# Optimization experiments

Measured on AMD Instinct MI355X. Metric: run time of the kernel, lower is better.

## Reference

```python
import jax, jax.numpy as jnp
import numpy as np


def setup_inputs() -> dict:
    key = jax.random.key(0)
    ks = jax.random.split(key, 6)
    B, T, I, H = 64, 4096, 128, 256
    x = jax.random.normal(ks[0], (B, T, I), dtype=jnp.float32)
    W_in = jax.random.normal(ks[1], (H, I), dtype=jnp.float32) * (1.0 / np.sqrt(I))
    b_in = jax.random.normal(ks[2], (H,), dtype=jnp.float32) * 0.01
    W_rec = jax.random.normal(ks[3], (H, H), dtype=jnp.float32) * (1.0 / np.sqrt(H))
    b_rec = jax.random.normal(ks[4], (H,), dtype=jnp.float32) * 0.01
    tau = jax.random.uniform(ks[5], (H,), dtype=jnp.float32)  # clamped to [0.1, 5] in forward
    return {"x": x, "W_in": W_in, "b_in": b_in, "W_rec": W_rec,
            "b_rec": b_rec, "tau": tau, "num_layers": 2}


def reference(x, W_in, b_in, W_rec, b_rec, tau, num_layers):
    # x: [B, T, I]; returns final hidden state h: [B, H]
    dt = jnp.float32(0.1)
    tau_c = jnp.clip(tau, 0.1, 5.0)                      # [H]
    scale = dt / tau_c                                   # [H]
    # Input projection is identical for every inner iteration -> precompute once.
    x_proj = jnp.einsum('bti,hi->bth', x, W_in) + b_in   # [B, T, H]
    B = x.shape[0]
    H = tau.shape[0]

    def step(h, xt):  # xt: [B, H]
        for _ in range(num_layers):  # small fixed inner loop
            act = jnp.tanh(xt + h @ W_rec.T + b_rec)
            h = h + scale * (act - h)
        return h, None

    h0 = jnp.zeros((B, H), dtype=x.dtype)
    h, _ = jax.lax.scan(step, h0, jnp.swapaxes(x_proj, 0, 1))  # scan over T
    return h
```

## Files before the change

kernel.cpp:

```cpp
#include <hip/hip_runtime.h>


typedef _Float16 half8 __attribute__((ext_vector_type(8)));
typedef float    f32x4 __attribute__((ext_vector_type(4)));

#define LGKM_BARRIER() asm volatile("s_waitcnt lgkmcnt(0)\n\ts_barrier" ::: "memory")

__device__ __forceinline__ half8 cvt8s(float4 v0, float4 v1, float s) {
    half8 hv;
    hv[0]=(_Float16)(v0.x*s); hv[1]=(_Float16)(v0.y*s);
    hv[2]=(_Float16)(v0.z*s); hv[3]=(_Float16)(v0.w*s);
    hv[4]=(_Float16)(v1.x*s); hv[5]=(_Float16)(v1.y*s);
    hv[6]=(_Float16)(v1.z*s); hv[7]=(_Float16)(v1.w*s);
    return hv;
}
__device__ __forceinline__ half8 cvt8(float4 v0, float4 v1) {
    half8 hv;
    hv[0]=(_Float16)v0.x; hv[1]=(_Float16)v0.y;
    hv[2]=(_Float16)v0.z; hv[3]=(_Float16)v0.w;
    hv[4]=(_Float16)v1.x; hv[5]=(_Float16)v1.y;
    hv[6]=(_Float16)v1.z; hv[7]=(_Float16)v1.w;
    return hv;
}

__global__ void __launch_bounds__(512, 2)
ltc_fused(const float* __restrict__ x,
          const float* __restrict__ W_in,
          const float* __restrict__ b_in,
          const float* __restrict__ W_rec,
          const float* __restrict__ b_rec,
          const float* __restrict__ tau,
          const int*   __restrict__ num_layers,
          float*       __restrict__ out,
          int T)
{
    const int b    = blockIdx.x;
    const int tid  = threadIdx.x;
    const int lane = tid & 63;
    const int g    = tid >> 6;
    const int n    = lane & 15;
    const int q    = lane >> 4;
    const int t_my = q & 1;
    const int L    = num_layers[0];
    const int mycol = 32*g + 16*t_my + n;
    const unsigned shamt = (unsigned)(t_my << 4);

    __shared__ _Float16 hbuf[2][256];
    __shared__ _Float16 xstage[2][16][16][8];
    __shared__ _Float16 pchunk[32][8][16][2];

    const float PRE = 2.8853900817779268f;
    half8 bh[2][8];
    half8 bx[2][4];
    float biasv[2];
#pragma unroll
    for (int t = 0; t < 2; ++t) {
        const int col = 32*g + 16*t + n;
        const float* rp = &W_rec[col * 256 + 8*q];
#pragma unroll
        for (int i = 0; i < 8; ++i)
            bh[t][i] = cvt8s(*(const float4*)&rp[32*i],
                             *(const float4*)&rp[32*i + 4], PRE);
        const float* ip = &W_in[col * 128 + 8*q];
#pragma unroll
        for (int i = 0; i < 4; ++i)
            bx[t][i] = cvt8s(*(const float4*)&ip[32*i],
                             *(const float4*)&ip[32*i + 4], PRE);
        biasv[t] = (b_in[col] + b_rec[col]) * PRE;
    }
    const float sj   = 0.1f / fminf(fmaxf(tau[mycol], 0.1f), 5.0f);
    const float nsj2 = -2.0f * sj;
    float hj = 0.0f;

    if (tid < 256) hbuf[0][tid] = (_Float16)0.0f;

    const float* xb  = x + (size_t)b * T * 128;
    const int    t_u = tid >> 4;
    const int    c16 = tid & 15;
    const int    Mts = t_u >> 4, ms = t_u & 15;

    float4 xpreA, xpreB;
    {
        int tg = t_u; if (tg > T - 1) tg = T - 1;
        const float4* src = (const float4*)(xb + (size_t)tg * 128 + 8*c16);
        xpreA = src[0]; xpreB = src[1];
    }

#define LAYER(RB, WB, XCQ)                                                   \
    do {                                                                     \
        half8 ah[8];                                                         \
        _Pragma("unroll")                                                    \
        for (int i = 0; i < 8; ++i)                                          \
            ah[i] = *(const half8*)&hbuf[RB][32*i + 8*q];                    \
        const float term1 = __builtin_fmaf(sj, 1.0f - hj, hj);               \
        const f32x4 zz = (f32x4){0.f, 0.f, 0.f, 0.f};                        \
        f32x4 A0[2], A1[2], A2[2], A3[2];                                    \
        _Pragma("unroll")                                                    \
        for (int t = 0; t < 2; ++t) {                                        \
            A0[t] = __builtin_amdgcn_mfma_f32_16x16x32_f16(                  \
                ah[0], bh[t][0], zz, 0, 0, 0);                               \
            A1[t] = __builtin_amdgcn_mfma_f32_16x16x32_f16(                  \
                ah[2], bh[t][2], zz, 0, 0, 0);                               \
            A2[t] = __builtin_amdgcn_mfma_f32_16x16x32_f16(                  \
                ah[4], bh[t][4], zz, 0, 0, 0);                               \
            A3[t] = __builtin_amdgcn_mfma_f32_16x16x32_f16(                  \
                ah[6], bh[t][6], zz, 0, 0, 0);                               \
        }                                                                    \
        _Pragma("unroll")                                                    \
        for (int t = 0; t < 2; ++t) {                                        \
            A0[t] = __builtin_amdgcn_mfma_f32_16x16x32_f16(                  \
                ah[1], bh[t][1], A0[t], 0, 0, 0);                            \
            A1[t] = __builtin_amdgcn_mfma_f32_16x16x32_f16(                  \
                ah[3], bh[t][3], A1[t], 0, 0, 0);                            \
            A2[t] = __builtin_amdgcn_mfma_f32_16x16x32_f16(                  \
                ah[5], bh[t][5], A2[t], 0, 0, 0);                            \
            A3[t] = __builtin_amdgcn_mfma_f32_16x16x32_f16(                  \
                ah[7], bh[t][7], A3[t], 0, 0, 0);                            \
        }                                                                    \
        float s0 = t_my ? A0[1][0] : A0[0][0];                               \
        float s1 = t_my ? A1[1][0] : A1[0][0];                               \
        float s2 = t_my ? A2[1][0] : A2[0][0];                               \
        float s3 = t_my ? A3[1][0] : A3[0][0];                               \
        float z  = ((s0 + s1) + (s2 + s3)) + (XCQ);                          \
        float e  = __builtin_amdgcn_exp2f(z);         \
        float rr = __builtin_amdgcn_rcpf(e + 1.0f);                          \
        hj = __builtin_fmaf(nsj2, rr, term1);            \
        hbuf[WB][mycol] = (_Float16)hj;  \
        LGKM_BARRIER();                                                      \
    } while (0)

#define STAGE_AND_PROJECT()                                                  \
    do {                                                                     \
        *(half8*)&xstage[Mts][c16][ms][0] = cvt8(xpreA, xpreB);              \
        __syncthreads();                                                     \
        _Pragma("unroll")                                                    \
        for (int Mt = 0; Mt < 2; ++Mt) {                                     \
            half8 ax[4];                                                     \
            _Pragma("unroll")                                                \
            for (int ks = 0; ks < 4; ++ks)                                   \
                ax[ks] = *(const half8*)&xstage[Mt][4*ks + q][n][0];         \
            f32x4 pa[2];                                                     \
            _Pragma("unroll")                                                \
            for (int t = 0; t < 2; ++t)                                      \
                pa[t] = (f32x4){biasv[t], biasv[t], biasv[t], biasv[t]};     \
            _Pragma("unroll")                                                \
            for (int ks = 0; ks < 4; ++ks)                                   \
                _Pragma("unroll")                                            \
                for (int t = 0; t < 2; ++t)                                  \
                    pa[t] = __builtin_amdgcn_mfma_f32_16x16x32_f16(          \
                        ax[ks], bx[t][ks], pa[t], 0, 0, 0);                  \
            _Pragma("unroll")                                                \
            for (int r = 0; r < 4; ++r) {                                    \
                union { _Float16 h[2]; unsigned u; } pk;                     \
                pk.h[0] = (_Float16)pa[0][r];                                \
                pk.h[1] = (_Float16)pa[1][r];                                \
                *(unsigned*)&pchunk[16*Mt + 4*q + r][g][n][0] = pk.u;        \
            }                                                                \
        }                                                                    \
        __syncthreads();                                                     \
    } while (0)

#define PREFETCH_NEXT()                                                      \
    do {                                                                     \
        const int nc = (tc + 32 < T) ? tc + 32 : tc;                         \
        int tg = nc + t_u; if (tg > T - 1) tg = T - 1;                       \
        const float4* src = (const float4*)(xb + (size_t)tg * 128 + 8*c16);  \
        xpreA = src[0]; xpreB = src[1];                                      \
    } while (0)

#define XCQ_LOAD(TS)                                                         \
    float xcq;                                                               \
    {                                                                        \
        unsigned d = *(const unsigned*)&pchunk[TS][g][n][0];                 \
        d >>= shamt;                                                         \
        union { unsigned u; _Float16 h[2]; } uu; uu.u = d;                   \
        xcq = (float)uu.h[0];                                                \
    }

    if (L == 2) {
        for (int tc = 0; tc < T; tc += 32) {
            STAGE_AND_PROJECT();
            PREFETCH_NEXT();
            const int tlen = (T - tc < 32) ? (T - tc) : 32;
#pragma unroll 2
            for (int ts = 0; ts < tlen; ++ts) {
                XCQ_LOAD(ts);
                LAYER(0, 1, xcq);
                LAYER(1, 0, xcq);
            }
        }
    } else {
        int hb = 0;
        for (int tc = 0; tc < T; tc += 32) {
            STAGE_AND_PROJECT();
            PREFETCH_NEXT();
            const int tlen = (T - tc < 32) ? (T - tc) : 32;
            for (int ts = 0; ts < tlen; ++ts) {
                XCQ_LOAD(ts);
                for (int l = 0; l < L; ++l) {
                    if (hb == 0) LAYER(0, 1, xcq);
                    else         LAYER(1, 0, xcq);
                    hb ^= 1;
                }
            }
        }
    }
#undef LAYER
#undef STAGE_AND_PROJECT
#undef PREFETCH_NEXT
#undef XCQ_LOAD

    if (q < 2)
        out[(size_t)b * 256 + mycol] = hj;
}

extern "C" void kernel_launch(void* const* d_in, const int* in_sizes, int n_in,
                              void* d_out, int out_size, void* d_ws, size_t ws_size,
                              hipStream_t stream) {
    const float* x     = (const float*)d_in[0];
    const float* W_in  = (const float*)d_in[1];
    const float* b_in  = (const float*)d_in[2];
    const float* W_rec = (const float*)d_in[3];
    const float* b_rec = (const float*)d_in[4];
    const float* tau   = (const float*)d_in[5];
    const int*   numl  = (const int*)d_in[6];

    const int H = in_sizes[2];
    const int I = in_sizes[1] / H;
    const int B = out_size / H;
    const int T = in_sizes[0] / (B * I);

    ltc_fused<<<B, 512, 0, stream>>>(x, W_in, b_in, W_rec, b_rec, tau,
                                     numl, (float*)d_out, T);
}
```

Measured before the change: 3.237 ms.

## Split recurrent matvec between MFMA waves and packed-dot VALU waves

Splits the 8 waves into two roles. Four waves each compute 32 of every 64 hidden columns with MFMA, and the other four compute the remaining columns with fdot2 dot products over register-resident fp16 W_rec halves, combined by a cross-lane shuffle. Column mapping and the projected-input lookup index are remapped to match. The aim is to halve the per-wave MFMA chain on the serial recurrence critical path, at the cost of 64 extra packed-weight registers and 16 LDS vector loads per VALU wave.

```diff
diff --git a/kernel.cpp b/kernel.cpp
--- a/kernel.cpp
+++ b/kernel.cpp
@@ -2,7 +2,10 @@
 
 
 typedef _Float16 half8 __attribute__((ext_vector_type(8)));
+typedef _Float16 h2    __attribute__((ext_vector_type(2)));
 typedef float    f32x4 __attribute__((ext_vector_type(4)));
+
+union H8u { half8 v; h2 p[4]; };
 
 #define LGKM_BARRIER() asm volatile("s_waitcnt lgkmcnt(0)\n\ts_barrier" ::: "memory")
 
@@ -41,8 +44,11 @@
     const int n    = lane & 15;
     const int q    = lane >> 4;
     const int t_my = q & 1;
+    const int p    = q >> 1;
+    const bool mfma_role = (g < 4);
     const int L    = num_layers[0];
-    const int mycol = 32*g + 16*t_my + n;
+    const int mycol = 64*(g & 3) + ((g >> 2) << 5) + (t_my << 4) + n;
+    const int pg    = mfma_role ? 2*g : 2*(g & 3) + 1;
     const unsigned shamt = (unsigned)(t_my << 4);
 
     __shared__ _Float16 hbuf[2][256];
@@ -50,17 +56,35 @@
     __shared__ _Float16 pchunk[32][8][16][2];
 
     const float PRE = 2.8853900817779268f;
+
     half8 bh[2][8];
+    h2    wv[64];
+    if (mfma_role) {
+#pragma unroll
+        for (int t = 0; t < 2; ++t) {
+            const int col = 64*g + 16*t + n;
+            const float* rp = &W_rec[col * 256 + 8*q];
+#pragma unroll
+            for (int i = 0; i < 8; ++i)
+                bh[t][i] = cvt8s(*(const float4*)&rp[32*i],
+                                 *(const float4*)&rp[32*i + 4], PRE);
+        }
+    } else {
+        const float* wp = &W_rec[mycol * 256 + 128*p];
+#pragma unroll
+        for (int j = 0; j < 32; ++j) {
+            float4 w4 = *(const float4*)&wp[4*j];
+            h2 a;  a[0]  = (_Float16)(w4.x * PRE); a[1]  = (_Float16)(w4.y * PRE);
+            h2 c2; c2[0] = (_Float16)(w4.z * PRE); c2[1] = (_Float16)(w4.w * PRE);
+            wv[2*j]   = a;
+            wv[2*j+1] = c2;
+        }
+    }
     half8 bx[2][4];
     float biasv[2];
 #pragma unroll
     for (int t = 0; t < 2; ++t) {
         const int col = 32*g + 16*t + n;
-        const float* rp = &W_rec[col * 256 + 8*q];
-#pragma unroll
-        for (int i = 0; i < 8; ++i)
-            bh[t][i] = cvt8s(*(const float4*)&rp[32*i],
-                             *(const float4*)&rp[32*i + 4], PRE);
         const float* ip = &W_in[col * 128 + 8*q];
 #pragma unroll
         for (int i = 0; i < 4; ++i)
@@ -88,44 +112,66 @@
 
 #define LAYER(RB, WB, XCQ)                                                   \
     do {                                                                     \
-        half8 ah[8];                                                         \
-        _Pragma("unroll")                                                    \
-        for (int i = 0; i < 8; ++i)                                          \
-            ah[i] = *(const half8*)&hbuf[RB][32*i + 8*q];                    \
+        float z;                                                             \
+        if (mfma_role) {                                                     \
+            half8 ah[8];                                                     \
+            _Pragma("unroll")                                                \
+            for (int i = 0; i < 8; ++i)                                      \
+                ah[i] = *(const half8*)&hbuf[RB][32*i + 8*q];                \
+            const f32x4 zz = (f32x4){0.f, 0.f, 0.f, 0.f};                    \
+            f32x4 A0[2], A1[2], A2[2], A3[2];                                \
+            _Pragma("unroll")                                                \
+            for (int t = 0; t < 2; ++t) {                                    \
+                A0[t] = __builtin_amdgcn_mfma_f32_16x16x32_f16(              \
+                    ah[0], bh[t][0], zz, 0, 0, 0);                           \
+                A1[t] = __builtin_amdgcn_mfma_f32_16x16x32_f16(              \
+                    ah[2], bh[t][2], zz, 0, 0, 0);                           \
+                A2[t] = __builtin_amdgcn_mfma_f32_16x16x32_f16(              \
+                    ah[4], bh[t][4], zz, 0, 0, 0);                           \
+                A3[t] = __builtin_amdgcn_mfma_f32_16x16x32_f16(              \
+                    ah[6], bh[t][6], zz, 0, 0, 0);                           \
+            }                                                                \
+            _Pragma("unroll")                                                \
+            for (int t = 0; t < 2; ++t) {                                    \
+                A0[t] = __builtin_amdgcn_mfma_f32_16x16x32_f16(              \
+                    ah[1], bh[t][1], A0[t], 0, 0, 0);                        \
+                A1[t] = __builtin_amdgcn_mfma_f32_16x16x32_f16(              \
+                    ah[3], bh[t][3], A1[t], 0, 0, 0);                        \
+                A2[t] = __builtin_amdgcn_mfma_f32_16x16x32_f16(              \
+                    ah[5], bh[t][5], A2[t], 0, 0, 0);                        \
+                A3[t] = __builtin_amdgcn_mfma_f32_16x16x32_f16(              \
+                    ah[7], bh[t][7], A3[t], 0, 0, 0);                        \
+            }                                                                \
+            float s0 = t_my ? A0[1][0] : A0[0][0];                           \
+            float s1 = t_my ? A1[1][0] : A1[0][0];                           \
+            float s2 = t_my ? A2[1][0] : A2[0][0];                           \
+            float s3 = t_my ? A3[1][0] : A3[0][0];                           \
+            z = ((s0 + s1) + (s2 + s3)) + (XCQ);                             \
+        } else {                                                             \
+            H8u hp[16];                                                      \
+            _Pragma("unroll")                                                \
+            for (int j = 0; j < 16; ++j)                                     \
+                hp[j].v = *(const half8*)&hbuf[RB][128*p + 8*j];             \
+            float acc0 = 0.f, acc1 = 0.f, acc2 = 0.f, acc3 = 0.f;            \
+            _Pragma("unroll")                                                \
+            for (int j = 0; j < 16; j += 4) {                                \
+                _Pragma("unroll")                                            \
+                for (int u = 0; u < 4; ++u) {                                \
+                    acc0 = __builtin_amdgcn_fdot2(hp[j  ].p[u], wv[4*j    +u], acc0, false); \
+                    acc1 = __builtin_amdgcn_fdot2(hp[j+1].p[u], wv[4*(j+1)+u], acc1, false); \
+                    acc2 = __builtin_amdgcn_fdot2(hp[j+2].p[u], wv[4*(j+2)+u], acc2, false); \
+                    acc3 = __builtin_amdgcn_fdot2(hp[j+3].p[u], wv[4*(j+3)+u], acc3, false); \
+                }                                                            \
+            }                                                                \
+            float sv = (acc0 + acc1) + (acc2 + acc3);                        \
+            float so = __shfl_xor(sv, 32);                                   \
+            z = (sv + so) + (XCQ);                                           \
+        }                                                                    \
         const float term1 = __builtin_fmaf(sj, 1.0f - hj, hj);               \
-        const f32x4 zz = (f32x4){0.f, 0.f, 0.f, 0.f};                        \
-        f32x4 A0[2], A1[2], A2[2], A3[2];                                    \
-        _Pragma("unroll")                                                    \
-        for (int t = 0; t < 2; ++t) {                                        \
-            A0[t] = __builtin_amdgcn_mfma_f32_16x16x32_f16(                  \
-                ah[0], bh[t][0], zz, 0, 0, 0);                               \
-            A1[t] = __builtin_amdgcn_mfma_f32_16x16x32_f16(                  \
-                ah[2], bh[t][2], zz, 0, 0, 0);                               \
-            A2[t] = __builtin_amdgcn_mfma_f32_16x16x32_f16(                  \
-                ah[4], bh[t][4], zz, 0, 0, 0);                               \
-            A3[t] = __builtin_amdgcn_mfma_f32_16x16x32_f16(                  \
-                ah[6], bh[t][6], zz, 0, 0, 0);                               \
-        }                                                                    \
-        _Pragma("unroll")                                                    \
-        for (int t = 0; t < 2; ++t) {                                        \
-            A0[t] = __builtin_amdgcn_mfma_f32_16x16x32_f16(                  \
-                ah[1], bh[t][1], A0[t], 0, 0, 0);                            \
-            A1[t] = __builtin_amdgcn_mfma_f32_16x16x32_f16(                  \
-                ah[3], bh[t][3], A1[t], 0, 0, 0);                            \
-            A2[t] = __builtin_amdgcn_mfma_f32_16x16x32_f16(                  \
-                ah[5], bh[t][5], A2[t], 0, 0, 0);                            \
-            A3[t] = __builtin_amdgcn_mfma_f32_16x16x32_f16(                  \
-                ah[7], bh[t][7], A3[t], 0, 0, 0);                            \
-        }                                                                    \
-        float s0 = t_my ? A0[1][0] : A0[0][0];                               \
-        float s1 = t_my ? A1[1][0] : A1[0][0];                               \
-        float s2 = t_my ? A2[1][0] : A2[0][0];                               \
-        float s3 = t_my ? A3[1][0] : A3[0][0];                               \
-        float z  = ((s0 + s1) + (s2 + s3)) + (XCQ);                          \
         float e  = __builtin_amdgcn_exp2f(z);         \
         float rr = __builtin_amdgcn_rcpf(e + 1.0f);                          \
         hj = __builtin_fmaf(nsj2, rr, term1);            \
-        hbuf[WB][mycol] = (_Float16)hj;  \
+        hbuf[WB][mycol] = (_Float16)hj;    \
         LGKM_BARRIER();                                                      \
     } while (0)
 
@@ -171,7 +217,7 @@
 #define XCQ_LOAD(TS)                                                         \
     float xcq;                                                               \
     {                                                                        \
-        unsigned d = *(const unsigned*)&pchunk[TS][g][n][0];                 \
+        unsigned d = *(const unsigned*)&pchunk[TS][pg][n][0];                \
         d >>= shamt;                                                         \
         union { unsigned u; _Float16 h[2]; } uu; uu.u = d;                   \
         xcq = (float)uu.h[0];                                                \
```

Result: slower. 4.493 ms (+38.8%).
